# Performance work log

Hardware: AMD Instinct MI355X
Metric: run time of the kernel (lower is better)

Reference implementation:

```python
import math
import jax, jax.numpy as jnp
import numpy as np

B, S, D = 1, 2048, 2048
H, KV, HD = 32, 4, 64  # n_heads, n_kv_heads, head_dim
N_REP = H // KV
ROPE_THETA = 10000.0


def setup_inputs() -> dict:
    key = jax.random.key(0)
    ks = jax.random.split(key, 6)
    x = jax.random.normal(ks[0], (B, S, D), dtype=jnp.float32)
    # precomputed rotary frequencies (real/imag parts of freqs_cis)
    inv_freq = 1.0 / (ROPE_THETA ** (jnp.arange(0, HD, 2, dtype=jnp.float32) / HD))  # [HD/2]
    t = jnp.arange(S, dtype=jnp.float32)
    ang = jnp.outer(t, inv_freq)  # [S, HD/2]
    freqs_cos = jnp.cos(ang)
    freqs_sin = jnp.sin(ang)
    # additive causal mask (large negative instead of -inf; numerically equivalent)
    mask = jnp.where(jnp.tril(jnp.ones((S, S), dtype=bool)), 0.0, -1e9).astype(jnp.float32)
    scale = 0.02
    wq = jax.random.normal(ks[1], (D, H * HD), dtype=jnp.float32) * scale
    wk = jax.random.normal(ks[2], (D, KV * HD), dtype=jnp.float32) * scale
    wv = jax.random.normal(ks[3], (D, KV * HD), dtype=jnp.float32) * scale
    wo = jax.random.normal(ks[4], (H * HD, D), dtype=jnp.float32) * scale
    return {"x": x, "freqs_cos": freqs_cos, "freqs_sin": freqs_sin, "mask": mask,
            "wq": wq, "wk": wk, "wv": wv, "wo": wo}


def _rope(t, cos, sin):
    # t: [B,S,h,HD]; cos/sin: [S, HD/2] -> complex multiply on (even, odd) pairs
    tr = t.reshape(*t.shape[:-1], HD // 2, 2)
    t0, t1 = tr[..., 0], tr[..., 1]
    c = cos[None, :, None, :]
    s = sin[None, :, None, :]
    o0 = t0 * c - t1 * s
    o1 = t0 * s + t1 * c
    return jnp.stack([o0, o1], axis=-1).reshape(t.shape)


def reference(x, freqs_cos, freqs_sin, mask, wq, wk, wv, wo):
    bsz, seqlen, _ = x.shape
    xq = (x @ wq).reshape(bsz, seqlen, H, HD)
    xk = (x @ wk).reshape(bsz, seqlen, KV, HD)
    xv = (x @ wv).reshape(bsz, seqlen, KV, HD)
    xq = _rope(xq, freqs_cos, freqs_sin)
    xk = _rope(xk, freqs_cos, freqs_sin)
    # GQA: repeat kv heads
    xk = jnp.repeat(xk, N_REP, axis=2)  # [B,S,H,HD]
    xv = jnp.repeat(xv, N_REP, axis=2)
    scores = jnp.einsum('bqhd,bkhd->bhqk', xq, xk) / math.sqrt(HD)
    scores = scores + mask[None, None, :, :]
    probs = jax.nn.softmax(scores.astype(jnp.float32), axis=-1).astype(xq.dtype)
    out = jnp.einsum('bhqk,bkhd->bqhd', probs, xv).reshape(bsz, seqlen, H * HD)
    return out @ wo
```

## Files before the change

kernel.cpp:

```cpp
#include <hip/hip_runtime.h>

typedef unsigned short u16;
typedef __attribute__((ext_vector_type(4))) float f32x4;
typedef __attribute__((ext_vector_type(16))) float f32x16;
typedef __attribute__((ext_vector_type(8))) short bf16x8;
typedef __attribute__((ext_vector_type(4))) unsigned short u16x4;
typedef __attribute__((ext_vector_type(4))) unsigned u32x4;
typedef __attribute__((ext_vector_type(2))) unsigned uv2;

__device__ __forceinline__ u16 f2bf(float f) {
  unsigned u = __float_as_uint(f);
  u += 0x7FFFu + ((u >> 16) & 1u);
  return (u16)(u >> 16);
}
__device__ __forceinline__ float bf2f(u16 v) {
  return __uint_as_float(((unsigned)v) << 16);
}

__device__ __forceinline__ void gload_lds16(const u16* g, u16* l) {
  __builtin_amdgcn_global_load_lds((const __attribute__((address_space(1))) void*)g,
                                   (__attribute__((address_space(3))) void*)l, 16, 0, 0);
}

__device__ __forceinline__ unsigned cvt_pk_bf16(float lo, float hi) {
  unsigned r;
  asm("v_cvt_pk_bf16_f32 %0, %1, %2" : "=v"(r) : "v"(lo), "v"(hi));
  return r;
}

__device__ __forceinline__ float fexp2(float x) {
#if __has_builtin(__builtin_amdgcn_exp2f)
  return __builtin_amdgcn_exp2f(x);
#else
  return __expf(x * 0.6931471805599453f);
#endif
}

__global__ __launch_bounds__(256) void convert_f32_bf16(const float* __restrict__ in,
                                                        u16* __restrict__ out, int n) {
  int i = (blockIdx.x * 256 + threadIdx.x) * 4;
  if (i >= n) return;
  float4 v = *(const float4*)&in[i];
  out[i + 0] = f2bf(v.x);
  out[i + 1] = f2bf(v.y);
  out[i + 2] = f2bf(v.z);
  out[i + 3] = f2bf(v.w);
}

__global__ __launch_bounds__(256) void transpose_f32_bf16(const float* __restrict__ in,
                                                          u16* __restrict__ out,
                                                          int R, int C) {
  __shared__ float tile[32][33];
  int c0 = blockIdx.x * 32, r0 = blockIdx.y * 32;
  int tx = threadIdx.x, ty = threadIdx.y;
  for (int j = 0; j < 32; j += 8)
    tile[ty + j][tx] = in[(size_t)(r0 + ty + j) * C + c0 + tx];
  __syncthreads();
  for (int j = 0; j < 32; j += 8)
    out[(size_t)(c0 + ty + j) * R + r0 + tx] = f2bf(tile[tx][ty + j]);
}

__global__ __launch_bounds__(256) void transpose_wqkv(const float* __restrict__ wq,
                                                      const float* __restrict__ wk,
                                                      const float* __restrict__ wv,
                                                      u16* __restrict__ out) {
  __shared__ float tile[32][33];
  int bx = blockIdx.x, r0 = blockIdx.y * 32;
  const float* src;
  int C, cc0;
  if (bx < 64) { src = wq; C = 2048; cc0 = bx * 32; }
  else if (bx < 72) { src = wk; C = 256; cc0 = (bx - 64) * 32; }
  else { src = wv; C = 256; cc0 = (bx - 72) * 32; }
  int tx = threadIdx.x, ty = threadIdx.y;
  for (int j = 0; j < 32; j += 8)
    tile[ty + j][tx] = src[(size_t)(r0 + ty + j) * C + cc0 + tx];
  __syncthreads();
  for (int j = 0; j < 32; j += 8)
    out[(size_t)(bx * 32 + ty + j) * 2048 + r0 + tx] = f2bf(tile[tx][ty + j]);
}

__global__ __launch_bounds__(256) void transpose_bf16(const u16* __restrict__ in, int ld_in,
                                                      u16* __restrict__ out, int R, int C) {
  __shared__ u16 tile[32][33];
  int c0 = blockIdx.x * 32, r0 = blockIdx.y * 32;
  int tx = threadIdx.x, ty = threadIdx.y;
  for (int j = 0; j < 32; j += 8)
    tile[ty + j][tx] = in[(size_t)(r0 + ty + j) * ld_in + c0 + tx];
  __syncthreads();
  for (int j = 0; j < 32; j += 8)
    out[(size_t)(c0 + ty + j) * R + r0 + tx] = tile[tx][ty + j];
}

template <bool F32OUT, bool DO_ROPE>
__global__ __launch_bounds__(512, 6) void gemm_bt(const u16* __restrict__ A,
                                                  const u16* __restrict__ BT,
                                                  void* __restrict__ Cout,
                                                  int M, int N, int K,
                                                  const float* __restrict__ cosT,
                                                  const float* __restrict__ sinT) {
  const int bn = blockIdx.x * 128, bm = blockIdx.y * 64;
  const int tid = threadIdx.x;
  const int wid = tid >> 6, lane = tid & 63;
  const int wr = wid >> 2, wc = wid & 3;
  const int lrow = lane & 15, g = lane >> 4;

  __shared__ __align__(16) u16 As[2][64 * 64];
  __shared__ __align__(16) u16 Bs[2][128 * 64];

  const int srow = tid >> 3;
  const int cswz = (((tid & 7) ^ (srow & 7)) << 3);
  const u16* a_src = A + (size_t)(bm + srow) * K + cswz;
  const u16* b_src = BT + (size_t)(bn + srow) * K + cswz;

  const int swz16 = (lrow & 7) << 3;
  const int colsw0 = (g * 8) ^ swz16;
  const int colsw1 = (32 + g * 8) ^ swz16;

#define STAGE(buf, k0)                                                        \
  do {                                                                        \
    gload_lds16(a_src + (k0), &As[buf][0] + tid * 8);                         \
    gload_lds16(b_src + (k0), &Bs[buf][0] + tid * 8);                         \
    gload_lds16(b_src + (size_t)64 * K + (k0), &Bs[buf][0] + 4096 + tid * 8); \
  } while (0)

  f32x4 acc[2][2] = {};

  const int nt = K >> 6;
  STAGE(0, 0);
  int cur = 0;
  for (int t = 0; t < nt; ++t) {
    if (t + 1 < nt) {
      STAGE(cur ^ 1, (t + 1) * 64);
      asm volatile("s_waitcnt vmcnt(3)" ::: "memory");
    } else {
      asm volatile("s_waitcnt vmcnt(0)" ::: "memory");
    }
    __builtin_amdgcn_s_barrier();
    asm volatile("" ::: "memory");

    bf16x8 af[2][2], bfr[2][2];
#pragma unroll
    for (int m = 0; m < 2; ++m) {
      int row = wr * 32 + m * 16 + lrow;
      af[m][0] = *(const bf16x8*)&As[cur][row * 64 + colsw0];
      af[m][1] = *(const bf16x8*)&As[cur][row * 64 + colsw1];
    }
#pragma unroll
    for (int n = 0; n < 2; ++n) {
      int row = wc * 32 + n * 16 + lrow;
      bfr[n][0] = *(const bf16x8*)&Bs[cur][row * 64 + colsw0];
      bfr[n][1] = *(const bf16x8*)&Bs[cur][row * 64 + colsw1];
    }
#pragma unroll
    for (int ks = 0; ks < 2; ++ks)
#pragma unroll
      for (int m = 0; m < 2; ++m)
#pragma unroll
        for (int n = 0; n < 2; ++n)
          acc[m][n] =
              __builtin_amdgcn_mfma_f32_16x16x32_bf16(af[m][ks], bfr[n][ks], acc[m][n], 0, 0, 0);

    asm volatile("" ::: "memory");
    __builtin_amdgcn_s_barrier();
    cur ^= 1;
  }
#undef STAGE

#pragma unroll
  for (int m = 0; m < 2; ++m) {
    int row0 = bm + wr * 32 + m * 16 + (g << 2);
#pragma unroll
    for (int n = 0; n < 2; ++n) {
      int col = bn + wc * 32 + n * 16 + lrow;
      f32x4 v = acc[m][n];
      if constexpr (DO_ROPE) {
        if (bn < 2304) {
          int i = (col & 63) >> 1;
          float sg = (col & 1) ? 1.f : -1.f;
#pragma unroll
          for (int r = 0; r < 4; ++r) {
            float pv = __shfl_xor(v[r], 1, 64);
            float c = cosT[(row0 + r) * 32 + i];
            float s = sinT[(row0 + r) * 32 + i];
            v[r] = v[r] * c + pv * s * sg;
          }
        }
      }
#pragma unroll
      for (int r = 0; r < 4; ++r) {
        if constexpr (F32OUT)
          ((float*)Cout)[(size_t)(row0 + r) * N + col] = v[r];
        else
          ((u16*)Cout)[(size_t)(row0 + r) * N + col] = f2bf(v[r]);
      }
    }
  }
}

__global__ __launch_bounds__(512) void attn_kernel(const u16* __restrict__ QKV,
                                                   const u16* __restrict__ VT,
                                                   u16* __restrict__ attn_out) {
  const int h = blockIdx.x;
  const int yy = (int)blockIdx.y;
  const int qb = (yy < 8) ? yy : 23 - yy;
  const int tid = threadIdx.x, w = tid >> 6, lane = tid & 63;
  const int wq4 = w & 3, half = w >> 2;
  const int l31 = lane & 31, hh = lane >> 5;
  const int kh = h >> 3;
  const int q0w = qb * 128 + wq4 * 32;
  const int qg = q0w + l31;

  __shared__ __align__(16) u16 smem[32768];

  const int srow8 = lane >> 3;
  const int scol = (((lane & 7) ^ srow8) << 3);

#define ASTAGE(buf, kb)                                                              \
  do {                                                                               \
    u16* kd = smem + (half * 2 + (buf)) * 4096 + (wq4 * 8) * 64 + lane * 8;          \
    u16* vd = smem + 16384 + (half * 2 + (buf)) * 4096 + (wq4 * 8) * 64 + lane * 8;  \
    _Pragma("unroll") for (int p = 0; p < 2; ++p) {                                  \
      int rr = p * 32 + wq4 * 8 + srow8;                                             \
      gload_lds16(QKV + (size_t)((kb) + rr) * 2560 + 2048 + kh * 64 + scol,          \
                  kd + p * 2048);                                                    \
      gload_lds16(VT + (size_t)(kh * 64 + rr) * 2048 + (kb) + scol, vd + p * 2048);  \
    }                                                                                \
  } while (0)

  bf16x8 qf[4];
  {
    size_t base = (size_t)qg * 2560 + h * 64 + hh * 8;
#pragma unroll
    for (int ks = 0; ks < 4; ++ks) qf[ks] = *(const bf16x8*)&QKV[base + ks * 16];
  }

  const int ksw = (l31 & 7) << 3;

  f32x16 acc0 = {}, acc1 = {};
  float mrun = -1e30f, lrun = 0.f;
  const float SC = 0.125f * 1.44269504088896f;

  const int NT = qb + 1;
  ASTAGE(0, half * 64);
  int cur = 0;

  for (int t = 0; t < NT; ++t) {
    const int kb = (2 * t + half) * 64;
    if (t + 1 < NT) {
      ASTAGE(cur ^ 1, kb + 128);
      asm volatile("s_waitcnt vmcnt(4)" ::: "memory");
    } else {
      asm volatile("s_waitcnt vmcnt(0)" ::: "memory");
    }
    __builtin_amdgcn_s_barrier();
    asm volatile("" ::: "memory");

    if (kb <= q0w + 31) {
      const u16* Kc = smem + (half * 2 + cur) * 4096;
      const u16* Vc = smem + 16384 + (half * 2 + cur) * 4096;

      f32x16 sc0 = {}, sc1 = {};
      __builtin_amdgcn_s_setprio(1);
#pragma unroll
      for (int ks = 0; ks < 4; ++ks) {
        int c = (ks * 16 + hh * 8) ^ ksw;
        bf16x8 kf0 = *(const bf16x8*)&Kc[l31 * 64 + c];
        bf16x8 kf1 = *(const bf16x8*)&Kc[(32 + l31) * 64 + c];
        sc0 = __builtin_amdgcn_mfma_f32_32x32x16_bf16(kf0, qf[ks], sc0, 0, 0, 0);
        sc1 = __builtin_amdgcn_mfma_f32_32x32x16_bf16(kf1, qf[ks], sc1, 0, 0, 0);
      }
      __builtin_amdgcn_s_setprio(0);

      if (kb + 63 > q0w) {
#pragma unroll
        for (int r = 0; r < 16; ++r) {
          int keyoff = (r & 3) + 8 * (r >> 2) + 4 * hh;
          if (kb + keyoff > qg) sc0[r] = -1e5f;
          if (kb + 32 + keyoff > qg) sc1[r] = -1e5f;
        }
      }

      float m8[8];
#pragma unroll
      for (int i = 0; i < 8; ++i)
        m8[i] = fmaxf(fmaxf(sc0[i], sc0[i + 8]), fmaxf(sc1[i], sc1[i + 8]));
#pragma unroll
      for (int st = 4; st >= 1; st >>= 1)
#pragma unroll
        for (int i = 0; i < st; ++i) m8[i] = fmaxf(m8[i], m8[i + st]);
      float mx = fmaxf(m8[0], __shfl_xor(m8[0], 32, 64));
      float mxs = mx * SC;

      if (__any(mxs > mrun + 8.f)) {
        float nm = fmaxf(mrun, mxs);
        float fs = fexp2(mrun - nm);
        mrun = nm;
        lrun *= fs;
#pragma unroll
        for (int i = 0; i < 16; ++i) { acc0[i] *= fs; acc1[i] *= fs; }
      }

      float p0[16], p1[16];
      const float nmn = -mrun;
#pragma unroll
      for (int i = 0; i < 16; ++i) {
        p0[i] = fexp2(__builtin_fmaf(sc0[i], SC, nmn));
        p1[i] = fexp2(__builtin_fmaf(sc1[i], SC, nmn));
      }
      float s8[8];
#pragma unroll
      for (int i = 0; i < 8; ++i) s8[i] = (p0[i] + p0[i + 8]) + (p1[i] + p1[i + 8]);
#pragma unroll
      for (int st = 4; st >= 1; st >>= 1)
#pragma unroll
        for (int i = 0; i < st; ++i) s8[i] += s8[i + st];
      lrun += s8[0] + __shfl_xor(s8[0], 32, 64);

      bf16x8 pf[4];
#pragma unroll
      for (int tt = 0; tt < 2; ++tt) {
        const float* pp = tt ? p1 : p0;
        unsigned wd[8];
#pragma unroll
        for (int j = 0; j < 8; ++j) wd[j] = cvt_pk_bf16(pp[2 * j], pp[2 * j + 1]);
        uv2 sA = __builtin_amdgcn_permlane32_swap(wd[0], wd[2], false, false);
        uv2 sB = __builtin_amdgcn_permlane32_swap(wd[1], wd[3], false, false);
        uv2 sC = __builtin_amdgcn_permlane32_swap(wd[4], wd[6], false, false);
        uv2 sD = __builtin_amdgcn_permlane32_swap(wd[5], wd[7], false, false);
        u32x4 f0 = {sA[0], sB[0], sA[1], sB[1]};
        u32x4 f1 = {sC[0], sD[0], sC[1], sD[1]};
        pf[tt * 2 + 0] = __builtin_bit_cast(bf16x8, f0);
        pf[tt * 2 + 1] = __builtin_bit_cast(bf16x8, f1);
      }

      __builtin_amdgcn_s_setprio(1);
#pragma unroll
      for (int ks = 0; ks < 4; ++ks) {
        int c = (ks * 16 + hh * 8) ^ ksw;
        bf16x8 vf0 = *(const bf16x8*)&Vc[l31 * 64 + c];
        bf16x8 vf1 = *(const bf16x8*)&Vc[(32 + l31) * 64 + c];
        acc0 = __builtin_amdgcn_mfma_f32_32x32x16_bf16(vf0, pf[ks], acc0, 0, 0, 0);
        acc1 = __builtin_amdgcn_mfma_f32_32x32x16_bf16(vf1, pf[ks], acc1, 0, 0, 0);
      }
      __builtin_amdgcn_s_setprio(0);
    }

    asm volatile("" ::: "memory");
    __builtin_amdgcn_s_barrier();
    cur ^= 1;
  }
#undef ASTAGE

  float* MRG = (float*)smem;
  float4* CH = (float4*)smem;
  if (half == 1) {
#pragma unroll
    for (int c = 0; c < 4; ++c) {
      float4 v0 = {acc0[4 * c + 0], acc0[4 * c + 1], acc0[4 * c + 2], acc0[4 * c + 3]};
      float4 v1 = {acc1[4 * c + 0], acc1[4 * c + 1], acc1[4 * c + 2], acc1[4 * c + 3]};
      CH[(wq4 * 8 + c) * 64 + lane] = v0;
      CH[(wq4 * 8 + 4 + c) * 64 + lane] = v1;
    }
    MRG[8192 + wq4 * 128 + lane * 2 + 0] = mrun;
    MRG[8192 + wq4 * 128 + lane * 2 + 1] = lrun;
  }
  __syncthreads();
  if (half == 0) {
    float m1 = MRG[8192 + wq4 * 128 + lane * 2 + 0];
    float l1 = MRG[8192 + wq4 * 128 + lane * 2 + 1];
    float m = fmaxf(mrun, m1);
    float f0 = fexp2(mrun - m), f1 = fexp2(m1 - m);
    float inv = 1.f / (lrun * f0 + l1 * f1);
    float a = f0 * inv, b = f1 * inv;
    size_t obase = (size_t)qg * 2048 + h * 64;
#pragma unroll
    for (int c = 0; c < 4; ++c) {
      float4 r0 = CH[(wq4 * 8 + c) * 64 + lane];
      float4 r1 = CH[(wq4 * 8 + 4 + c) * 64 + lane];
      u16x4 o0, o1;
      o0[0] = f2bf(acc0[4 * c + 0] * a + r0.x * b);
      o0[1] = f2bf(acc0[4 * c + 1] * a + r0.y * b);
      o0[2] = f2bf(acc0[4 * c + 2] * a + r0.z * b);
      o0[3] = f2bf(acc0[4 * c + 3] * a + r0.w * b);
      o1[0] = f2bf(acc1[4 * c + 0] * a + r1.x * b);
      o1[1] = f2bf(acc1[4 * c + 1] * a + r1.y * b);
      o1[2] = f2bf(acc1[4 * c + 2] * a + r1.z * b);
      o1[3] = f2bf(acc1[4 * c + 3] * a + r1.w * b);
      *(u16x4*)&attn_out[obase + 8 * c + 4 * hh] = o0;
      *(u16x4*)&attn_out[obase + 32 + 8 * c + 4 * hh] = o1;
    }
  }
}

extern "C" void kernel_launch(void* const* d_in, const int* in_sizes, int n_in,
                              void* d_out, int out_size, void* d_ws, size_t ws_size,
                              hipStream_t stream) {
  const float* x = (const float*)d_in[0];
  const float* fcos = (const float*)d_in[1];
  const float* fsin = (const float*)d_in[2];
  const float* wq = (const float*)d_in[4];
  const float* wk = (const float*)d_in[5];
  const float* wv = (const float*)d_in[6];
  const float* wo = (const float*)d_in[7];

  char* ws = (char*)d_ws;
  u16* xb    = (u16*)(ws);
  u16* wqkvT = (u16*)(ws + (8u << 20));
  u16* woT   = (u16*)(ws + (18u << 20));
  u16* QKV   = (u16*)(ws + (26u << 20));
  u16* VT    = (u16*)(ws + (36u << 20));
  u16* attn  = xb;

  dim3 tb32(32, 8);

  convert_f32_bf16<<<4096, 256, 0, stream>>>(x, xb, 2048 * 2048);
  transpose_wqkv<<<dim3(80, 64), tb32, 0, stream>>>(wq, wk, wv, wqkvT);
  transpose_f32_bf16<<<dim3(64, 64), tb32, 0, stream>>>(wo, woT, 2048, 2048);

  gemm_bt<false, true><<<dim3(20, 32), 512, 0, stream>>>(xb, wqkvT, QKV, 2048, 2560, 2048,
                                                         fcos, fsin);

  transpose_bf16<<<dim3(8, 64), tb32, 0, stream>>>(QKV + 2304, 2560, VT, 2048, 256);

  attn_kernel<<<dim3(32, 16), 512, 0, stream>>>(QKV, VT, attn);

  gemm_bt<true, false><<<dim3(16, 32), 512, 0, stream>>>(attn, woT, d_out, 2048, 2048, 2048,
                                                         nullptr, nullptr);
}
```

Measured before the change: 115.2 us.

## Fuse weight/input prep kernels and load V fragments directly from global in attention

Merges the three preprocessing kernels (x conversion, Wqkv transpose, Wo transpose) into one launch with vectorized float4 loads and u16x4 stores. This is meant to cut launch overhead and improve memory coalescing. In the attention kernel, V tiles are no longer staged through LDS; each lane loads its V^T fragments straight from global memory into registers at the top of the iteration. That shrinks LDS and lowers the vmcnt wait threshold, but uncoalesced per-lane global loads may add latency that the pipeline no longer hides.

```diff
diff --git a/kernel.cpp b/kernel.cpp
--- a/kernel.cpp
+++ b/kernel.cpp
@@ -36,47 +36,59 @@
 #endif
 }
 
-__global__ __launch_bounds__(256) void convert_f32_bf16(const float* __restrict__ in,
-                                                        u16* __restrict__ out, int n) {
-  int i = (blockIdx.x * 256 + threadIdx.x) * 4;
-  if (i >= n) return;
-  float4 v = *(const float4*)&in[i];
-  out[i + 0] = f2bf(v.x);
-  out[i + 1] = f2bf(v.y);
-  out[i + 2] = f2bf(v.z);
-  out[i + 3] = f2bf(v.w);
-}
-
-__global__ __launch_bounds__(256) void transpose_f32_bf16(const float* __restrict__ in,
-                                                          u16* __restrict__ out,
-                                                          int R, int C) {
+__global__ __launch_bounds__(256) void prep_fused(const float* __restrict__ x,
+                                                  const float* __restrict__ wq,
+                                                  const float* __restrict__ wk,
+                                                  const float* __restrict__ wv,
+                                                  const float* __restrict__ wo,
+                                                  u16* __restrict__ xb,
+                                                  u16* __restrict__ wqkvT,
+                                                  u16* __restrict__ woT) {
+  const int b = blockIdx.x, tid = threadIdx.x;
+  if (b < 2048) {
+    int i = (b * 256 + tid) * 8;
+    float4 v0 = *(const float4*)&x[i];
+    float4 v1 = *(const float4*)&x[i + 4];
+    u16x4 o0 = {f2bf(v0.x), f2bf(v0.y), f2bf(v0.z), f2bf(v0.w)};
+    u16x4 o1 = {f2bf(v1.x), f2bf(v1.y), f2bf(v1.z), f2bf(v1.w)};
+    *(u16x4*)&xb[i] = o0;
+    *(u16x4*)&xb[i + 4] = o1;
+    return;
+  }
   __shared__ float tile[32][33];
-  int c0 = blockIdx.x * 32, r0 = blockIdx.y * 32;
-  int tx = threadIdx.x, ty = threadIdx.y;
-  for (int j = 0; j < 32; j += 8)
-    tile[ty + j][tx] = in[(size_t)(r0 + ty + j) * C + c0 + tx];
+  int tb = b - 2048;
+  const float* src;
+  u16* dst;
+  int C, nbase, r0, c0;
+  if (tb < 4096) {
+    src = wq; dst = wqkvT; C = 2048;
+    c0 = (tb >> 6) * 32; r0 = (tb & 63) * 32; nbase = c0;
+  } else if (tb < 4608) {
+    tb -= 4096; src = wk; dst = wqkvT; C = 256;
+    c0 = (tb >> 6) * 32; r0 = (tb & 63) * 32; nbase = 2048 + c0;
+  } else if (tb < 5120) {
+    tb -= 4608; src = wv; dst = wqkvT; C = 256;
+    c0 = (tb >> 6) * 32; r0 = (tb & 63) * 32; nbase = 2304 + c0;
+  } else {
+    tb -= 5120; src = wo; dst = woT; C = 2048;
+    c0 = (tb >> 6) * 32; r0 = (tb & 63) * 32; nbase = c0;
+  }
+  {
+    int tr = tid >> 3, tc4 = (tid & 7) << 2;
+    float4 v = *(const float4*)&src[(size_t)(r0 + tr) * C + c0 + tc4];
+    tile[tr][tc4 + 0] = v.x;
+    tile[tr][tc4 + 1] = v.y;
+    tile[tr][tc4 + 2] = v.z;
+    tile[tr][tc4 + 3] = v.w;
+  }
   __syncthreads();
-  for (int j = 0; j < 32; j += 8)
-    out[(size_t)(c0 + ty + j) * R + r0 + tx] = f2bf(tile[tx][ty + j]);
-}
-
-__global__ __launch_bounds__(256) void transpose_wqkv(const float* __restrict__ wq,
-                                                      const float* __restrict__ wk,
-                                                      const float* __restrict__ wv,
-                                                      u16* __restrict__ out) {
-  __shared__ float tile[32][33];
-  int bx = blockIdx.x, r0 = blockIdx.y * 32;
-  const float* src;
-  int C, cc0;
-  if (bx < 64) { src = wq; C = 2048; cc0 = bx * 32; }
-  else if (bx < 72) { src = wk; C = 256; cc0 = (bx - 64) * 32; }
-  else { src = wv; C = 256; cc0 = (bx - 72) * 32; }
-  int tx = threadIdx.x, ty = threadIdx.y;
-  for (int j = 0; j < 32; j += 8)
-    tile[ty + j][tx] = src[(size_t)(r0 + ty + j) * C + cc0 + tx];
-  __syncthreads();
-  for (int j = 0; j < 32; j += 8)
-    out[(size_t)(bx * 32 + ty + j) * 2048 + r0 + tx] = f2bf(tile[tx][ty + j]);
+  {
+    int orow = tid >> 3, oc = (tid & 7) << 2;
+    u16x4 o;
+#pragma unroll
+    for (int e = 0; e < 4; ++e) o[e] = f2bf(tile[oc + e][orow]);
+    *(u16x4*)&dst[(size_t)(nbase + orow) * 2048 + r0 + oc] = o;
+  }
 }
 
 __global__ __launch_bounds__(256) void transpose_bf16(const u16* __restrict__ in, int ld_in,
@@ -210,7 +222,7 @@
   const int q0w = qb * 128 + wq4 * 32;
   const int qg = q0w + l31;
 
-  __shared__ __align__(16) u16 smem[32768];
+  __shared__ __align__(16) u16 smem[18432];
 
   const int srow8 = lane >> 3;
   const int scol = (((lane & 7) ^ srow8) << 3);
@@ -218,12 +230,10 @@
 #define ASTAGE(buf, kb)                                                              \
   do {                                                                               \
     u16* kd = smem + (half * 2 + (buf)) * 4096 + (wq4 * 8) * 64 + lane * 8;          \
-    u16* vd = smem + 16384 + (half * 2 + (buf)) * 4096 + (wq4 * 8) * 64 + lane * 8;  \
     _Pragma("unroll") for (int p = 0; p < 2; ++p) {                                  \
       int rr = p * 32 + wq4 * 8 + srow8;                                             \
       gload_lds16(QKV + (size_t)((kb) + rr) * 2560 + 2048 + kh * 64 + scol,          \
                   kd + p * 2048);                                                    \
-      gload_lds16(VT + (size_t)(kh * 64 + rr) * 2048 + (kb) + scol, vd + p * 2048);  \
     }                                                                                \
   } while (0)
 
@@ -235,6 +245,8 @@
   }
 
   const int ksw = (l31 & 7) << 3;
+  const u16* vrow0 = VT + (size_t)(kh * 64 + l31) * 2048 + hh * 8;
+  const u16* vrow1 = VT + (size_t)(kh * 64 + 32 + l31) * 2048 + hh * 8;
 
   f32x16 acc0 = {}, acc1 = {};
   float mrun = -1e30f, lrun = 0.f;
@@ -246,18 +258,28 @@
 
   for (int t = 0; t < NT; ++t) {
     const int kb = (2 * t + half) * 64;
+    const bool act = (kb <= q0w + 31);
+
+    bf16x8 vf0[4], vf1[4];
+    if (act) {
+#pragma unroll
+      for (int ks = 0; ks < 4; ++ks) {
+        vf0[ks] = *(const bf16x8*)&vrow0[kb + ks * 16];
+        vf1[ks] = *(const bf16x8*)&vrow1[kb + ks * 16];
+      }
+    }
+
     if (t + 1 < NT) {
       ASTAGE(cur ^ 1, kb + 128);
-      asm volatile("s_waitcnt vmcnt(4)" ::: "memory");
+      asm volatile("s_waitcnt vmcnt(2)" ::: "memory");
     } else {
       asm volatile("s_waitcnt vmcnt(0)" ::: "memory");
     }
     __builtin_amdgcn_s_barrier();
     asm volatile("" ::: "memory");
 
-    if (kb <= q0w + 31) {
+    if (act) {
       const u16* Kc = smem + (half * 2 + cur) * 4096;
-      const u16* Vc = smem + 16384 + (half * 2 + cur) * 4096;
 
       f32x16 sc0 = {}, sc1 = {};
       __builtin_amdgcn_s_setprio(1);
@@ -336,11 +358,8 @@
       __builtin_amdgcn_s_setprio(1);
 #pragma unroll
       for (int ks = 0; ks < 4; ++ks) {
-        int c = (ks * 16 + hh * 8) ^ ksw;
-        bf16x8 vf0 = *(const bf16x8*)&Vc[l31 * 64 + c];
-        bf16x8 vf1 = *(const bf16x8*)&Vc[(32 + l31) * 64 + c];
-        acc0 = __builtin_amdgcn_mfma_f32_32x32x16_bf16(vf0, pf[ks], acc0, 0, 0, 0);
-        acc1 = __builtin_amdgcn_mfma_f32_32x32x16_bf16(vf1, pf[ks], acc1, 0, 0, 0);
+        acc0 = __builtin_amdgcn_mfma_f32_32x32x16_bf16(vf0[ks], pf[ks], acc0, 0, 0, 0);
+        acc1 = __builtin_amdgcn_mfma_f32_32x32x16_bf16(vf1[ks], pf[ks], acc1, 0, 0, 0);
       }
       __builtin_amdgcn_s_setprio(0);
     }
@@ -413,9 +432,7 @@
 
   dim3 tb32(32, 8);
 
-  convert_f32_bf16<<<4096, 256, 0, stream>>>(x, xb, 2048 * 2048);
-  transpose_wqkv<<<dim3(80, 64), tb32, 0, stream>>>(wq, wk, wv, wqkvT);
-  transpose_f32_bf16<<<dim3(64, 64), tb32, 0, stream>>>(wo, woT, 2048, 2048);
+  prep_fused<<<11264, 256, 0, stream>>>(x, wq, wk, wv, wo, xb, wqkvT, woT);
 
   gemm_bt<false, true><<<dim3(20, 32), 512, 0, stream>>>(xb, wqkvT, QKV, 2048, 2560, 2048,
                                                          fcos, fsin);
```

Result: slower. 143.0 us (+24.1%).
